# Kernel tuning notes

Hardware: AMD Instinct MI355X
Metric: run time of the kernel (lower is better)

The kernel has to match this reference:

```python
import jax, jax.numpy as jnp
import numpy as np

B, S, E = 2, 2048, 1024
H, KV = 16, 4
D = E // H            # head_dim = 64
N_REP = H // KV       # 4
WIN = 256             # window_size
KV_DIM = KV * D       # 256


def setup_inputs() -> dict:
    key = jax.random.key(0)
    ks = jax.random.split(key, 10)
    sc_e = 1.0 / np.sqrt(E)
    return {
        "x":  jax.random.normal(ks[0], (B, S, E), jnp.float32),
        # weights stored as [in, out] (transposed torch Linear weight)
        "wq": jax.random.normal(ks[1], (E, E), jnp.float32) * sc_e,
        "bq": jax.random.normal(ks[2], (E,), jnp.float32) * 0.01,
        "wk": jax.random.normal(ks[3], (E, KV_DIM), jnp.float32) * sc_e,
        "bk": jax.random.normal(ks[4], (KV_DIM,), jnp.float32) * 0.01,
        "wv": jax.random.normal(ks[5], (E, KV_DIM), jnp.float32) * sc_e,
        "bv": jax.random.normal(ks[6], (KV_DIM,), jnp.float32) * 0.01,
        "wo": jax.random.normal(ks[7], (E, E), jnp.float32) * sc_e,
        "bo": jax.random.normal(ks[8], (E,), jnp.float32) * 0.01,
    }


def reference(x, wq, bq, wk, bk, wv, bv, wo, bo):
    b, s, _ = x.shape
    q = (x @ wq + bq).reshape(b, s, H, D).transpose(0, 2, 1, 3)    # [B,H,S,D]
    k = (x @ wk + bk).reshape(b, s, KV, D).transpose(0, 2, 1, 3)   # [B,KV,S,D]
    v = (x @ wv + bv).reshape(b, s, KV, D).transpose(0, 2, 1, 3)
    # repeat_kv: each kv head repeated N_REP times consecutively
    k = jnp.repeat(k, N_REP, axis=1)                               # [B,H,S,D]
    v = jnp.repeat(v, N_REP, axis=1)
    scores = jnp.einsum("bhqd,bhkd->bhqk", q, k) * (D ** -0.5)    # [B,H,S,S]
    i = jnp.arange(s)[:, None]
    j = jnp.arange(s)[None, :]
    masked = (j > i) | ((i - j) > WIN)  # True = masked (causal sliding window)
    scores = jnp.where(masked[None, None], -jnp.inf, scores)
    attn = jax.nn.softmax(scores, axis=-1)
    ctx = jnp.einsum("bhqk,bhkd->bhqd", attn, v)                   # [B,H,S,D]
    ctx = ctx.transpose(0, 2, 1, 3).reshape(b, s, E)
    return ctx @ wo + bo
```

## Files before the change

### kernel.cpp

```cpp
#include <hip/hip_runtime.h>
#include <stdint.h>

typedef unsigned short u16;
typedef __attribute__((ext_vector_type(8))) __bf16 bf16x8;
typedef __attribute__((ext_vector_type(4))) __bf16 bf16x4;
typedef __attribute__((ext_vector_type(4))) float f32x4;

#define S_LEN 2048
#define EMB   1024
#define NH    16
#define NKV   4
#define HD    64
#define WIN   256
#define NB    2
#define MROWS (NB * S_LEN)
#define PPAD  72

__device__ __forceinline__ u16 f2bf(float f) {
    uint32_t u = __float_as_uint(f);
    uint32_t r = (u + 0x7FFFu + ((u >> 16) & 1u)) >> 16;
    return (u16)r;
}

__device__ __forceinline__ float fast_exp2(float x) {
#if __has_builtin(__builtin_amdgcn_exp2f)
    return __builtin_amdgcn_exp2f(x);
#else
    float r; asm("v_exp_f32 %0, %1" : "=v"(r) : "v"(x)); return r;
#endif
}

__device__ __forceinline__ void gload16(const void* g, void* l) {
    __builtin_amdgcn_global_load_lds(
        (const __attribute__((address_space(1))) uint32_t*)(uintptr_t)g,
        (__attribute__((address_space(3))) uint32_t*)(uintptr_t)l,
        16, 0, 0);
}

__device__ __forceinline__ void transpose_job64(const float* __restrict__ in,
                                                u16* __restrict__ out,
                                                int R, int C, int bx, int by, int tid) {
    __shared__ float t[64][33];
    int c0 = bx * 32, r0 = by * 64;
    int tx = tid & 31, ty = tid >> 5;
#pragma unroll
    for (int j = 0; j < 64; j += 8)
        t[ty + j][tx] = in[(size_t)(r0 + ty + j) * C + (c0 + tx)];
    __syncthreads();
#pragma unroll
    for (int j = 0; j < 32; j += 8) {
        int c = j + ty;
        uint32_t v = f2bf(t[2 * tx][c]) | ((uint32_t)f2bf(t[2 * tx + 1][c]) << 16);
        *(uint32_t*)(out + (size_t)(c0 + c) * R + r0 + 2 * tx) = v;
    }
}

__global__ __launch_bounds__(256) void prep_kernel(
    const float* __restrict__ x,  const float* __restrict__ wq,
    const float* __restrict__ wk, const float* __restrict__ wv,
    const float* __restrict__ wo,
    u16* __restrict__ xb, u16* __restrict__ wqt, u16* __restrict__ wkt,
    u16* __restrict__ wvt, u16* __restrict__ wot) {
    int bid = blockIdx.x, tid = threadIdx.x;
    if (bid < 2048) {
        int i = bid * 256 + tid;
        const float4* p = (const float4*)x + (size_t)i * 2;
        float4 a = p[0], b = p[1];
        uint4 q;
        q.x = f2bf(a.x) | ((uint32_t)f2bf(a.y) << 16);
        q.y = f2bf(a.z) | ((uint32_t)f2bf(a.w) << 16);
        q.z = f2bf(b.x) | ((uint32_t)f2bf(b.y) << 16);
        q.w = f2bf(b.z) | ((uint32_t)f2bf(b.w) << 16);
        ((uint4*)xb)[i] = q;
    } else if (bid < 2560) {
        int lb = bid - 2048;  transpose_job64(wq, wqt, EMB, EMB, lb & 31, lb >> 5, tid);
    } else if (bid < 2688) {
        int lb = bid - 2560;  transpose_job64(wk, wkt, EMB, 256, lb & 7, lb >> 3, tid);
    } else if (bid < 2816) {
        int lb = bid - 2688;  transpose_job64(wv, wvt, EMB, 256, lb & 7, lb >> 3, tid);
    } else {
        int lb = bid - 2816;  transpose_job64(wo, wot, EMB, EMB, lb & 31, lb >> 5, tid);
    }
}

__device__ __forceinline__ void gemm_core64(const __bf16* __restrict__ A, const __bf16* __restrict__ Bt,
                                            int K, int m0, int n0r,
                                            __bf16 (*As)[64 * 64], __bf16 (*Bs)[128 * 64],
                                            f32x4 (&acc)[2][4], int tid) {
    const int lane = tid & 63, w = tid >> 6;
    const int wr = w >> 1, wc = w & 1;
    const int r = lane & 15, g = lane >> 4;

    auto stage = [&](int buf, int k0) {
#pragma unroll
        for (int i = 0; i < 2; ++i) {
            int chunk = (w * 2 + i) * 64 + lane;
            int row = chunk >> 3, cc = chunk & 7;
            gload16(A + (size_t)(m0 + row) * K + k0 + cc * 8, &As[buf][(w * 2 + i) * 512]);
        }
#pragma unroll
        for (int i = 0; i < 4; ++i) {
            int chunk = (w * 4 + i) * 64 + lane;
            int row = chunk >> 3, cc = chunk & 7;
            gload16(Bt + (size_t)(n0r + row) * K + k0 + cc * 8, &Bs[buf][(w * 4 + i) * 512]);
        }
    };

    stage(0, 0);
    __syncthreads();
    for (int k0 = 0; k0 < K; k0 += 64) {
        int cur = (k0 >> 6) & 1;
        if (k0 + 64 < K) stage(cur ^ 1, k0 + 64);
        bf16x8 af[2][2], bfr[4][2];
#pragma unroll
        for (int mf = 0; mf < 2; ++mf)
#pragma unroll
            for (int kk = 0; kk < 2; ++kk)
                af[mf][kk] = *(const bf16x8*)(&As[cur][(wr * 32 + mf * 16 + r) * 64 + kk * 32 + g * 8]);
#pragma unroll
        for (int nf = 0; nf < 4; ++nf)
#pragma unroll
            for (int kk = 0; kk < 2; ++kk)
                bfr[nf][kk] = *(const bf16x8*)(&Bs[cur][(wc * 64 + nf * 16 + r) * 64 + kk * 32 + g * 8]);
#pragma unroll
        for (int mf = 0; mf < 2; ++mf)
#pragma unroll
            for (int nf = 0; nf < 4; ++nf)
#pragma unroll
                for (int kk = 0; kk < 2; ++kk)
                    acc[mf][nf] = __builtin_amdgcn_mfma_f32_16x16x32_bf16(
                        af[mf][kk], bfr[nf][kk], acc[mf][nf], 0, 0, 0);
        __syncthreads();
    }
}

__global__ __launch_bounds__(256, 3) void gemm_qkv_kernel(
    const __bf16* __restrict__ xb, const __bf16* __restrict__ wqt,
    const __bf16* __restrict__ wkt, const __bf16* __restrict__ wvt,
    const float* __restrict__ bq, const float* __restrict__ bk, const float* __restrict__ bv,
    __bf16* __restrict__ Qb, __bf16* __restrict__ Kb, __bf16* __restrict__ Vblk) {
    __shared__ __align__(16) __bf16 As[2][64 * 64];
    __shared__ __align__(16) __bf16 Bs[2][128 * 64];
    int tid = threadIdx.x;
    int wg = (blockIdx.x & 7) * 96 + (blockIdx.x >> 3);
    int n0 = (wg % 12) * 128, m0 = (wg / 12) * 64;

    const __bf16* Bt; int n0r; const float* bias; int mode;
    if (n0 < 1024)      { Bt = wqt; n0r = n0;        bias = bq; mode = 0; }
    else if (n0 < 1280) { Bt = wkt; n0r = n0 - 1024; bias = bk; mode = 1; }
    else                { Bt = wvt; n0r = n0 - 1280; bias = bv; mode = 2; }

    f32x4 acc[2][4];
    f32x4 z = {0.f, 0.f, 0.f, 0.f};
#pragma unroll
    for (int i = 0; i < 2; ++i)
#pragma unroll
        for (int j = 0; j < 4; ++j) acc[i][j] = z;

    gemm_core64(xb, Bt, EMB, m0, n0r, As, Bs, acc, tid);

    const int lane = tid & 63, w = tid >> 6;
    const int wr = w >> 1, wc = w & 1, r = lane & 15, g = lane >> 4;
#pragma unroll
    for (int nf = 0; nf < 4; ++nf) {
        int nn = n0r + wc * 64 + nf * 16 + r;
        float bb = bias[nn];
        int hh = nn >> 6, dd = nn & 63;
        if (mode == 2) {
#pragma unroll
            for (int mf = 0; mf < 2; ++mf) {
                int s0 = m0 + wr * 32 + mf * 16 + g * 4;
                int bi = s0 >> 11, s = s0 & 2047;
                bf16x4 pk;
#pragma unroll
                for (int reg = 0; reg < 4; ++reg) pk[reg] = (__bf16)(acc[mf][nf][reg] + bb);
                *reinterpret_cast<bf16x4*>(Vblk + (size_t)(bi * NKV + hh) * (S_LEN * HD)
                                           + (s >> 6) * 4096 + dd * 64 + (s & 63)) = pk;
            }
        } else {
#pragma unroll
            for (int mf = 0; mf < 2; ++mf)
#pragma unroll
                for (int reg = 0; reg < 4; ++reg) {
                    int m = m0 + wr * 32 + mf * 16 + g * 4 + reg;
                    int bi = m >> 11, s = m & 2047;
                    __bf16 o = (__bf16)(acc[mf][nf][reg] + bb);
                    if (mode == 0)
                        Qb[((size_t)(bi * NH + hh) * S_LEN + s) * HD + dd] = o;
                    else
                        Kb[((size_t)(bi * NKV + hh) * S_LEN + s) * HD + dd] = o;
                }
        }
    }
}

__global__ __launch_bounds__(256, 3) void attn_kernel(const __bf16* __restrict__ Qb,
                                                      const __bf16* __restrict__ Kb,
                                                      const __bf16* __restrict__ Vblk,
                                                      __bf16* __restrict__ ctx) {
    __shared__ __align__(16) __bf16 Ks[2][64 * 64];
    __shared__ __align__(16) __bf16 Vs[2][64 * 64];
    __shared__ __align__(16) __bf16 Plds[4][32 * PPAD];
    const int tid = threadIdx.x;
    const int lane = tid & 63, w = tid >> 6;
    const int r = lane & 15, g = lane >> 4;
    const int q0 = blockIdx.x * 128;
    const int h = blockIdx.y, b = blockIdx.z;
    const int kvh = h >> 2;
    const __bf16* Kh = Kb + (size_t)(b * NKV + kvh) * S_LEN * HD;
    const __bf16* Vh = Vblk + (size_t)(b * NKV + kvh) * S_LEN * HD;
    __bf16* Pw = &Plds[w][0];

    const int n0s = w * 128 + lane;
    const int n1s = n0s + 64;
    const int srcoff0 = (n0s >> 3) * 64 + (((n0s & 7) ^ ((n0s >> 3) & 7)) * 8);
    const int srcoff1 = (n1s >> 3) * 64 + (((n1s & 7) ^ ((n1s >> 3) & 7)) * 8);
    const int dst0 = (w * 2) * 512;
    const int dst1 = dst0 + 512;

    auto stage = [&](int buf, int kbase) {
        const __bf16* Kt = Kh + (size_t)kbase * 64;
        const __bf16* Vt = Vh + (size_t)kbase * 64;
        gload16(Kt + srcoff0, &Ks[buf][dst0]);
        gload16(Kt + srcoff1, &Ks[buf][dst1]);
        gload16(Vt + srcoff0, &Vs[buf][dst0]);
        gload16(Vt + srcoff1, &Vs[buf][dst1]);
    };

    const int swz0 = ((0 * 4 + g) ^ (r & 7)) * 8;
    const int swz1 = ((1 * 4 + g) ^ (r & 7)) * 8;

    bf16x8 qf[2][2];
#pragma unroll
    for (int gq = 0; gq < 2; ++gq)
#pragma unroll
        for (int kk = 0; kk < 2; ++kk)
            qf[gq][kk] = *(const bf16x8*)(Qb + ((size_t)(b * NH + h) * S_LEN
                                          + q0 + w * 32 + gq * 16 + r) * HD + kk * 32 + g * 8);

    f32x4 z = {0.f, 0.f, 0.f, 0.f};
    f32x4 o[2][4];
#pragma unroll
    for (int gq = 0; gq < 2; ++gq)
#pragma unroll
        for (int i = 0; i < 4; ++i) o[gq][i] = z;
    float psum[2] = {0.f, 0.f};

    const float SC = 0.18033688011112042f;
    int iq[2];
#pragma unroll
    for (int gq = 0; gq < 2; ++gq) iq[gq] = q0 + w * 32 + gq * 16 + r;

    auto tile = [&](int buf, int kbase) {
        const __bf16* Kl = &Ks[buf][0];
        const __bf16* Vl = &Vs[buf][0];
        f32x4 sa[2][4];
#pragma unroll
        for (int gq = 0; gq < 2; ++gq)
#pragma unroll
            for (int nf = 0; nf < 4; ++nf) sa[gq][nf] = z;
#pragma unroll
        for (int nf = 0; nf < 4; ++nf) {
            bf16x8 kf0 = *(const bf16x8*)(Kl + nf * 1024 + r * 64 + swz0);
            bf16x8 kf1 = *(const bf16x8*)(Kl + nf * 1024 + r * 64 + swz1);
            sa[0][nf] = __builtin_amdgcn_mfma_f32_16x16x32_bf16(kf0, qf[0][0], sa[0][nf], 0, 0, 0);
            sa[1][nf] = __builtin_amdgcn_mfma_f32_16x16x32_bf16(kf0, qf[1][0], sa[1][nf], 0, 0, 0);
            sa[0][nf] = __builtin_amdgcn_mfma_f32_16x16x32_bf16(kf1, qf[0][1], sa[0][nf], 0, 0, 0);
            sa[1][nf] = __builtin_amdgcn_mfma_f32_16x16x32_bf16(kf1, qf[1][1], sa[1][nf], 0, 0, 0);
        }
#pragma unroll
        for (int gq = 0; gq < 2; ++gq)
#pragma unroll
            for (int nf = 0; nf < 4; ++nf) {
                int jb = kbase + nf * 16 + g * 4;
                bf16x4 pk;
#pragma unroll
                for (int reg = 0; reg < 4; ++reg) {
                    float x = sa[gq][nf][reg] * SC;
                    uint32_t d = (uint32_t)(iq[gq] - (jb + reg));
                    x = (d <= (uint32_t)WIN) ? x : -1e30f;
                    float e = fast_exp2(x);
                    psum[gq] += e;
                    pk[reg] = (__bf16)e;
                }
                *reinterpret_cast<bf16x4*>(Pw + gq * 16 * PPAD + r * PPAD + nf * 16 + g * 4) = pk;
            }
#pragma unroll
        for (int kk2 = 0; kk2 < 2; ++kk2) {
            bf16x8 pa0 = *(const bf16x8*)(Pw + r * PPAD + kk2 * 32 + g * 8);
            bf16x8 pa1 = *(const bf16x8*)(Pw + 16 * PPAD + r * PPAD + kk2 * 32 + g * 8);
            int sw = kk2 ? swz1 : swz0;
#pragma unroll
            for (int nf2 = 0; nf2 < 4; ++nf2) {
                bf16x8 vf = *(const bf16x8*)(Vl + nf2 * 1024 + r * 64 + sw);
                o[0][nf2] = __builtin_amdgcn_mfma_f32_16x16x32_bf16(vf, pa0, o[0][nf2], 0, 0, 0);
                o[1][nf2] = __builtin_amdgcn_mfma_f32_16x16x32_bf16(vf, pa1, o[1][nf2], 0, 0, 0);
            }
        }
    };

    const int kb0 = (q0 >= 256) ? (q0 - 256) : 0;
    const int nt = (q0 + 64 - kb0) / 64 + 1;
    stage(0, kb0);
    __syncthreads();
    for (int t = 0; t < nt; ++t) {
        int kbase = kb0 + t * 64;
        if (t + 1 < nt) stage((t + 1) & 1, kbase + 64);
        tile(t & 1, kbase);
        __syncthreads();
    }

#pragma unroll
    for (int gq = 0; gq < 2; ++gq) {
        psum[gq] += __shfl_xor(psum[gq], 16, 64);
        psum[gq] += __shfl_xor(psum[gq], 32, 64);
        float linv = 1.0f / psum[gq];
        int s = q0 + w * 32 + gq * 16 + r;
#pragma unroll
        for (int nf2 = 0; nf2 < 4; ++nf2) {
            bf16x4 pk;
#pragma unroll
            for (int reg = 0; reg < 4; ++reg) pk[reg] = (__bf16)(o[gq][nf2][reg] * linv);
            *reinterpret_cast<bf16x4*>(ctx + ((size_t)(b * S_LEN + s)) * EMB
                                       + h * 64 + nf2 * 16 + g * 4) = pk;
        }
    }
}

__global__ __launch_bounds__(256, 3) void gemm_out_kernel(const __bf16* __restrict__ ctxb,
                                                          const __bf16* __restrict__ wot,
                                                          const float* __restrict__ bo,
                                                          float* __restrict__ out) {
    __shared__ __align__(16) __bf16 As[2][64 * 64];
    __shared__ __align__(16) __bf16 Bs[2][128 * 64];
    int tid = threadIdx.x;
    int wg = (blockIdx.x & 7) * 64 + (blockIdx.x >> 3);
    int n0 = (wg % 8) * 128, m0 = (wg / 8) * 64;

    f32x4 acc[2][4];
    f32x4 z = {0.f, 0.f, 0.f, 0.f};
#pragma unroll
    for (int i = 0; i < 2; ++i)
#pragma unroll
        for (int j = 0; j < 4; ++j) acc[i][j] = z;

    gemm_core64(ctxb, wot, EMB, m0, n0, As, Bs, acc, tid);

    const int lane = tid & 63, w = tid >> 6;
    const int wr = w >> 1, wc = w & 1, r = lane & 15, g = lane >> 4;
#pragma unroll
    for (int nf = 0; nf < 4; ++nf) {
        int n = n0 + wc * 64 + nf * 16 + r;
        float bb = bo[n];
#pragma unroll
        for (int mf = 0; mf < 2; ++mf)
#pragma unroll
            for (int reg = 0; reg < 4; ++reg) {
                int m = m0 + wr * 32 + mf * 16 + g * 4 + reg;
                out[(size_t)m * EMB + n] = acc[mf][nf][reg] + bb;
            }
    }
}

extern "C" void kernel_launch(void* const* d_in, const int* in_sizes, int n_in,
                              void* d_out, int out_size, void* d_ws, size_t ws_size,
                              hipStream_t stream) {
    const float* x  = (const float*)d_in[0];
    const float* wq = (const float*)d_in[1];
    const float* bq = (const float*)d_in[2];
    const float* wk = (const float*)d_in[3];
    const float* bk = (const float*)d_in[4];
    const float* wv = (const float*)d_in[5];
    const float* bv = (const float*)d_in[6];
    const float* wo = (const float*)d_in[7];
    const float* bo = (const float*)d_in[8];
    float* out = (float*)d_out;

    char* ws = (char*)d_ws;
    __bf16* xb   = (__bf16*)ws;          ws += (size_t)MROWS * EMB * 2;
    __bf16* wqt  = (__bf16*)ws;          ws += (size_t)EMB * EMB * 2;
    __bf16* wkt  = (__bf16*)ws;          ws += (size_t)256 * EMB * 2;
    __bf16* wvt  = (__bf16*)ws;          ws += (size_t)256 * EMB * 2;
    __bf16* wot  = (__bf16*)ws;          ws += (size_t)EMB * EMB * 2;
    __bf16* Qb   = (__bf16*)ws;          ws += (size_t)NB * NH * S_LEN * HD * 2;
    __bf16* Kb   = (__bf16*)ws;          ws += (size_t)NB * NKV * S_LEN * HD * 2;
    __bf16* Vblk = (__bf16*)ws;          ws += (size_t)NB * NKV * S_LEN * HD * 2;
    __bf16* ctx  = (__bf16*)ws;          ws += (size_t)MROWS * EMB * 2;

    prep_kernel<<<3328, 256, 0, stream>>>(x, wq, wk, wv, wo,
                                          (u16*)xb, (u16*)wqt, (u16*)wkt, (u16*)wvt, (u16*)wot);
    gemm_qkv_kernel<<<768, 256, 0, stream>>>(xb, wqt, wkt, wvt, bq, bk, bv, Qb, Kb, Vblk);
    attn_kernel<<<dim3(16, 16, 2), 256, 0, stream>>>(Qb, Kb, Vblk, ctx);
    gemm_out_kernel<<<512, 256, 0, stream>>>(ctx, wot, bo, out);
}
```

Measured before the change: 66.16 us.

## Move wo transpose into attention kernel and skip fully-masked warp tiles

The wo weight transpose moves out of the prep kernel and into 256 extra blocks appended to the attention launch, so it runs alongside attention and shortens the prep stage on the critical path. Each extra block reuses the K shared-memory buffer as transpose scratch. The attention loop also lets warps skip the first or last KV tile when those rows are entirely masked by the sliding window or causal bound. This lowers MFMA work, at the cost of more blocks competing for attention occupancy.

```diff
diff --git a/kernel.cpp b/kernel.cpp
--- a/kernel.cpp
+++ b/kernel.cpp
@@ -39,8 +39,8 @@
 
 __device__ __forceinline__ void transpose_job64(const float* __restrict__ in,
                                                 u16* __restrict__ out,
-                                                int R, int C, int bx, int by, int tid) {
-    __shared__ float t[64][33];
+                                                int R, int C, int bx, int by, int tid,
+                                                float (*t)[33]) {
     int c0 = bx * 32, r0 = by * 64;
     int tx = tid & 31, ty = tid >> 5;
 #pragma unroll
@@ -58,9 +58,9 @@
 __global__ __launch_bounds__(256) void prep_kernel(
     const float* __restrict__ x,  const float* __restrict__ wq,
     const float* __restrict__ wk, const float* __restrict__ wv,
-    const float* __restrict__ wo,
     u16* __restrict__ xb, u16* __restrict__ wqt, u16* __restrict__ wkt,
-    u16* __restrict__ wvt, u16* __restrict__ wot) {
+    u16* __restrict__ wvt) {
+    __shared__ float t[64][33];
     int bid = blockIdx.x, tid = threadIdx.x;
     if (bid < 2048) {
         int i = bid * 256 + tid;
@@ -73,13 +73,11 @@
         q.w = f2bf(b.z) | ((uint32_t)f2bf(b.w) << 16);
         ((uint4*)xb)[i] = q;
     } else if (bid < 2560) {
-        int lb = bid - 2048;  transpose_job64(wq, wqt, EMB, EMB, lb & 31, lb >> 5, tid);
+        int lb = bid - 2048;  transpose_job64(wq, wqt, EMB, EMB, lb & 31, lb >> 5, tid, t);
     } else if (bid < 2688) {
-        int lb = bid - 2560;  transpose_job64(wk, wkt, EMB, 256, lb & 7, lb >> 3, tid);
-    } else if (bid < 2816) {
-        int lb = bid - 2688;  transpose_job64(wv, wvt, EMB, 256, lb & 7, lb >> 3, tid);
+        int lb = bid - 2560;  transpose_job64(wk, wkt, EMB, 256, lb & 7, lb >> 3, tid, t);
     } else {
-        int lb = bid - 2816;  transpose_job64(wo, wot, EMB, EMB, lb & 31, lb >> 5, tid);
+        int lb = bid - 2688;  transpose_job64(wv, wvt, EMB, 256, lb & 7, lb >> 3, tid, t);
     }
 }
 
@@ -197,15 +195,29 @@
 __global__ __launch_bounds__(256, 3) void attn_kernel(const __bf16* __restrict__ Qb,
                                                       const __bf16* __restrict__ Kb,
                                                       const __bf16* __restrict__ Vblk,
+                                                      const float* __restrict__ wo,
+                                                      u16* __restrict__ wot,
                                                       __bf16* __restrict__ ctx) {
     __shared__ __align__(16) __bf16 Ks[2][64 * 64];
     __shared__ __align__(16) __bf16 Vs[2][64 * 64];
     __shared__ __align__(16) __bf16 Plds[4][32 * PPAD];
     const int tid = threadIdx.x;
+    const int bid = blockIdx.x;
+
+    if (bid >= 512) {
+        float (*t)[33] = reinterpret_cast<float(*)[33]>(&Ks[0][0]);
+        int j0 = (bid - 512) * 2;
+        transpose_job64(wo, wot, EMB, EMB, j0 & 31, j0 >> 5, tid, t);
+        __syncthreads();
+        int j1 = j0 + 1;
+        transpose_job64(wo, wot, EMB, EMB, j1 & 31, j1 >> 5, tid, t);
+        return;
+    }
+
     const int lane = tid & 63, w = tid >> 6;
     const int r = lane & 15, g = lane >> 4;
-    const int q0 = blockIdx.x * 128;
-    const int h = blockIdx.y, b = blockIdx.z;
+    const int q0 = (bid & 15) * 128;
+    const int h = (bid >> 4) & 15, b = bid >> 8;
     const int kvh = h >> 2;
     const __bf16* Kh = Kb + (size_t)(b * NKV + kvh) * S_LEN * HD;
     const __bf16* Vh = Vblk + (size_t)(b * NKV + kvh) * S_LEN * HD;
@@ -303,10 +315,11 @@
     const int nt = (q0 + 64 - kb0) / 64 + 1;
     stage(0, kb0);
     __syncthreads();
-    for (int t = 0; t < nt; ++t) {
-        int kbase = kb0 + t * 64;
-        if (t + 1 < nt) stage((t + 1) & 1, kbase + 64);
-        tile(t & 1, kbase);
+    for (int tt = 0; tt < nt; ++tt) {
+        int kbase = kb0 + tt * 64;
+        if (tt + 1 < nt) stage((tt + 1) & 1, kbase + 64);
+        bool skip = (tt == 0 && q0 >= 256 && w >= 2) || (tt == nt - 1 && w < 2);
+        if (!skip) tile(tt & 1, kbase);
         __syncthreads();
     }
 
@@ -387,9 +400,9 @@
     __bf16* Vblk = (__bf16*)ws;          ws += (size_t)NB * NKV * S_LEN * HD * 2;
     __bf16* ctx  = (__bf16*)ws;          ws += (size_t)MROWS * EMB * 2;
 
-    prep_kernel<<<3328, 256, 0, stream>>>(x, wq, wk, wv, wo,
-                                          (u16*)xb, (u16*)wqt, (u16*)wkt, (u16*)wvt, (u16*)wot);
+    prep_kernel<<<2816, 256, 0, stream>>>(x, wq, wk, wv,
+                                          (u16*)xb, (u16*)wqt, (u16*)wkt, (u16*)wvt);
     gemm_qkv_kernel<<<768, 256, 0, stream>>>(xb, wqt, wkt, wvt, bq, bk, bv, Qb, Kb, Vblk);
-    attn_kernel<<<dim3(16, 16, 2), 256, 0, stream>>>(Qb, Kb, Vblk, ctx);
+    attn_kernel<<<768, 256, 0, stream>>>(Qb, Kb, Vblk, wo, (u16*)wot, ctx);
     gemm_out_kernel<<<512, 256, 0, stream>>>(ctx, wot, bo, out);
 }
```

After: 63.90 us, median of 3. 3.4% less time.
